# Kernel optimization log

Hardware: AMD Instinct MI355X
Metric: run time of the kernel (lower is better)

The kernel has to match this reference:

```python
import jax, jax.numpy as jnp
import numpy as np

D_MODEL = 1024
NUM_HEADS = 16
HEAD_DIM = D_MODEL // NUM_HEADS
B, S = 2, 2048


def setup_inputs() -> dict:
    key = jax.random.key(0)
    ks = jax.random.split(key, 12)
    s = 1.0 / np.sqrt(D_MODEL)
    return {
        "query": jax.random.normal(ks[0], (B, S, D_MODEL), jnp.float32),
        "key": jax.random.normal(ks[1], (B, S, D_MODEL), jnp.float32),
        "value": jax.random.normal(ks[2], (B, S, D_MODEL), jnp.float32),
        "attn_mask": jnp.ones((B, 1, 1, S), dtype=bool),
        "w_q": jax.random.uniform(ks[3], (D_MODEL, D_MODEL), jnp.float32, -s, s),
        "b_q": jax.random.uniform(ks[4], (D_MODEL,), jnp.float32, -s, s),
        "w_k": jax.random.uniform(ks[5], (D_MODEL, D_MODEL), jnp.float32, -s, s),
        "b_k": jax.random.uniform(ks[6], (D_MODEL,), jnp.float32, -s, s),
        "w_v": jax.random.uniform(ks[7], (D_MODEL, D_MODEL), jnp.float32, -s, s),
        "b_v": jax.random.uniform(ks[8], (D_MODEL,), jnp.float32, -s, s),
        "w_o": jax.random.uniform(ks[9], (D_MODEL, D_MODEL), jnp.float32, -s, s),
        "b_o": jax.random.uniform(ks[10], (D_MODEL,), jnp.float32, -s, s),
    }


def _split_heads(x):
    b, s, _ = x.shape
    return x.reshape(b, s, NUM_HEADS, HEAD_DIM).transpose(0, 2, 1, 3)  # [B,H,S,hd]


def reference(query, key, value, attn_mask, w_q, b_q, w_k, b_k, w_v, b_v, w_o, b_o):
    q = _split_heads(query @ w_q.T + b_q)
    k = _split_heads(key @ w_k.T + b_k)
    v = _split_heads(value @ w_v.T + b_v)
    scale = 1.0 / np.sqrt(HEAD_DIM).astype(np.float32)
    scores = jnp.einsum("bhqd,bhkd->bhqk", q, k) * scale  # [B,H,S,S]
    scores = jnp.where(attn_mask, scores, jnp.float32(-1e9))
    weights = jax.nn.softmax(scores, axis=-1)
    attended = jnp.einsum("bhqk,bhkd->bhqd", weights, v)
    merged = attended.transpose(0, 2, 1, 3).reshape(query.shape[0], query.shape[1], D_MODEL)
    return merged @ w_o.T + b_o
```

## Files before the change

kernel.cpp:

```cpp
#include <hip/hip_runtime.h>

#define D_MODEL 1024
#define NHEADS 16
#define HDIM 64
#define BATCH 2
#define SEQ 2048

typedef __attribute__((ext_vector_type(8))) short short8;
typedef __attribute__((ext_vector_type(4))) float floatx4;

__device__ __forceinline__ short f2bf(float f) {
    unsigned u = __builtin_bit_cast(unsigned, f);
    u += 0x7fffu + ((u >> 16) & 1u);
    return (short)(u >> 16);
}

#if defined(__has_builtin)
#if __has_builtin(__builtin_amdgcn_cvt_pk_bf16_f32)
#define HAS_PK_BF16 1
#endif
#if __has_builtin(__builtin_amdgcn_exp2f)
#define EXP2(x) __builtin_amdgcn_exp2f(x)
#endif
#endif
#ifndef EXP2
#define EXP2(x) exp2f(x)
#endif
__device__ __forceinline__ unsigned pk2bf(float a, float b) {
#ifdef HAS_PK_BF16
    auto r = __builtin_amdgcn_cvt_pk_bf16_f32(a, b);
    unsigned out;
    __builtin_memcpy(&out, &r, 4);
    return out;
#else
    unsigned ua = __builtin_bit_cast(unsigned, a);
    ua += 0x7fffu + ((ua >> 16) & 1u);
    unsigned ub = __builtin_bit_cast(unsigned, b);
    ub += 0x7fffu + ((ub >> 16) & 1u);
    return (ua >> 16) | (ub & 0xffff0000u);
#endif
}

__device__ __forceinline__ void gll16(const void* g, void* l) {
    __builtin_amdgcn_global_load_lds(
        (const __attribute__((address_space(1))) unsigned int*)g,
        (__attribute__((address_space(3))) unsigned int*)l, 16, 0, 0);
}

__global__ __launch_bounds__(256)
void cvt_all(const float* __restrict__ q, const float* __restrict__ k,
             const float* __restrict__ v, const float* __restrict__ wq,
             const float* __restrict__ wk, const float* __restrict__ wv,
             const float* __restrict__ wo, short* __restrict__ ws)
{
    const int seg = blockIdx.y;
    const float* src; short* dst; int n;
    const int M4 = 1 << 22, M1 = 1 << 20;
    switch (seg) {
        case 0: src = q;  dst = ws;                    n = M4; break;
        case 1: src = k;  dst = ws + M4;               n = M4; break;
        case 2: src = v;  dst = ws + 2 * M4;           n = M4; break;
        case 3: src = wq; dst = ws + 3 * M4;           n = M1; break;
        case 4: src = wk; dst = ws + 3 * M4 + M1;      n = M1; break;
        case 5: src = wv; dst = ws + 3 * M4 + 2 * M1;  n = M1; break;
        default:src = wo; dst = ws + 3 * M4 + 3 * M1;  n = M1; break;
    }
    int idx = (blockIdx.x * 256 + threadIdx.x) * 8;
    if (idx >= n) return;
    float4 f0 = *(const float4*)(src + idx);
    float4 f1 = *(const float4*)(src + idx + 4);
    uint4 o = { pk2bf(f0.x, f0.y), pk2bf(f0.z, f0.w),
                pk2bf(f1.x, f1.y), pk2bf(f1.z, f1.w) };
    *(uint4*)(dst + idx) = o;
}

template<int FINAL>
__global__ __launch_bounds__(256)
void gemm_pipe(const short* __restrict__ Abase, const short* __restrict__ Wbase,
               const float* __restrict__ b0, const float* __restrict__ b1,
               const float* __restrict__ b2, void* __restrict__ outp,
               float scale0)
{
    constexpr int BM = FINAL ? 64 : 128;
    constexpr int WM = FINAL ? 32 : 64;
    constexpr int MT = WM / 16;
    constexpr int AG = BM / 32;
    __shared__ short smem[BM * 64 + 128 * 64];
    short* As = smem;
    short* Bs = smem + BM * 64;

    const int tid  = threadIdx.x;
    const int lane = tid & 63;
    const int w    = tid >> 6;
    const int wr   = (w >> 1) * WM;
    const int wc   = (w & 1) * 64;
    const int m0   = blockIdx.y * BM;
    const int n0   = blockIdx.x * 128;
    const int z    = FINAL ? 0 : blockIdx.z;

    const short* A = Abase + (size_t)z * (1 << 22);
    const short* W = Wbase + (size_t)z * (1 << 20);
    const float* bias = FINAL ? b0 : (z == 0 ? b0 : (z == 1 ? b1 : b2));
    const float scale = (!FINAL && z == 0) ? scale0 : 1.0f;

    const int slr = lane >> 3;
    const int scb = (lane & 7) ^ slr;
    const int fm  = lane & 15;
    const int fq  = lane >> 4;

    const short* aSrc[AG];
    const short* bSrc[4];
#pragma unroll
    for (int i = 0; i < AG; ++i)
        aSrc[i] = A + (size_t)(m0 + (w * AG + i) * 8 + slr) * D_MODEL + scb * 8;
#pragma unroll
    for (int i = 0; i < 4; ++i)
        bSrc[i] = W + (size_t)(n0 + (w * 4 + i) * 8 + slr) * D_MODEL + scb * 8;

    short8 pa[AG], pb[4];
#pragma unroll
    for (int i = 0; i < AG; ++i) pa[i] = *(const short8*)(aSrc[i]);
#pragma unroll
    for (int i = 0; i < 4; ++i)  pb[i] = *(const short8*)(bSrc[i]);

    floatx4 acc[MT][4] = {};

    for (int k0 = 0; k0 < D_MODEL; k0 += 64) {
        __syncthreads();
#pragma unroll
        for (int i = 0; i < AG; ++i)
            *(short8*)(As + (w * AG + i) * 512 + lane * 8) = pa[i];
#pragma unroll
        for (int i = 0; i < 4; ++i)
            *(short8*)(Bs + (w * 4 + i) * 512 + lane * 8) = pb[i];
        const int kn = (k0 + 64) & (D_MODEL - 1);
#pragma unroll
        for (int i = 0; i < AG; ++i) pa[i] = *(const short8*)(aSrc[i] + kn);
#pragma unroll
        for (int i = 0; i < 4; ++i)  pb[i] = *(const short8*)(bSrc[i] + kn);
        __syncthreads();

#pragma unroll
        for (int ks = 0; ks < 2; ++ks) {
            short8 af[MT], bfv[4];
#pragma unroll
            for (int mt = 0; mt < MT; ++mt) {
                int row = wr + mt * 16 + fm;
                af[mt] = *(const short8*)(As + row * 64 + ((ks * 4 + fq) ^ (row & 7)) * 8);
            }
#pragma unroll
            for (int nt = 0; nt < 4; ++nt) {
                int row = wc + nt * 16 + fm;
                bfv[nt] = *(const short8*)(Bs + row * 64 + ((ks * 4 + fq) ^ (row & 7)) * 8);
            }
#pragma unroll
            for (int mt = 0; mt < MT; ++mt)
#pragma unroll
                for (int nt = 0; nt < 4; ++nt)
                    acc[mt][nt] = __builtin_amdgcn_mfma_f32_16x16x32_bf16(
                        af[mt], bfv[nt], acc[mt][nt], 0, 0, 0);
        }
    }

    if (!FINAL && z == 2) {
        __syncthreads();
        short* T = smem;
#pragma unroll
        for (int nt = 0; nt < 4; ++nt) {
            int nl = wc + nt * 16 + fm;
            float bv = bias[n0 + nl];
#pragma unroll
            for (int mt = 0; mt < MT; ++mt)
#pragma unroll
                for (int r = 0; r < 4; ++r) {
                    int m = wr + mt * 16 + fq * 4 + r;
                    int mp = (m & 64) | ((m & 15) << 2) | ((m >> 4) & 3);
                    T[nl * 128 + (((mp >> 3) ^ (nl & 15)) << 3) + (mp & 7)]
                        = f2bf(acc[mt][nt][r] + bv);
                }
        }
        __syncthreads();
        const int nl   = tid >> 1, half = tid & 1;
        const int gb   = m0 >> 11;
        const int gh   = (n0 + nl) >> 6, gd = (n0 + nl) & 63;
        const int ms   = m0 & 2047;
        short* gdst = (short*)outp + ((size_t)2 << 22)
                    + ((((size_t)(gb * NHEADS + gh)) << 6) + gd) * SEQ + ms;
#pragma unroll
        for (int c = 0; c < 8; ++c) {
            int lc = half * 8 + c;
            int p  = lc ^ (nl & 15);
            *(short8*)(gdst + lc * 8) = *(const short8*)(T + nl * 128 + p * 8);
        }
        return;
    }
#pragma unroll
    for (int nt = 0; nt < 4; ++nt) {
        int n = n0 + wc + nt * 16 + fm;
        float bv = bias[n];
#pragma unroll
        for (int mt = 0; mt < MT; ++mt) {
#pragma unroll
            for (int r = 0; r < 4; ++r) {
                int m = m0 + wr + mt * 16 + fq * 4 + r;
                float val = (acc[mt][nt][r] + bv) * scale;
                if (FINAL) {
                    ((float*)outp)[(size_t)m * D_MODEL + n] = val;
                } else {
                    short* outz = (short*)outp + (size_t)z * (1 << 22);
                    int b = m >> 11, s = m & 2047, h = n >> 6, d = n & 63;
                    outz[(((size_t)(b * NHEADS + h) * SEQ + s) << 6) + d] = f2bf(val);
                }
            }
        }
    }
}

__global__ __launch_bounds__(256, 4)
void flash5(const short* __restrict__ qh, const short* __restrict__ kh,
            const short* __restrict__ vT, short* __restrict__ ab)
{
    __shared__ short Ks[2 * 64 * 64];
    __shared__ short Vt[2 * 64 * 64];
    __shared__ short Ps[64 * 64];

    const int tid  = threadIdx.x;
    const int lane = tid & 63;
    const int w    = tid >> 6;
    const int wq0  = w * 16;
    const int bh   = blockIdx.y;
    const int b    = bh >> 4, h = bh & 15;
    const int s0   = blockIdx.x * 64;
    const size_t base = (size_t)bh << 17;

    const int fm = lane & 15;
    const int fq = lane >> 4;
    const int fk = fq * 8;

    short8 qf[2];
#pragma unroll
    for (int ks = 0; ks < 2; ++ks)
        qf[ks] = *(const short8*)(qh + base +
            (size_t)(s0 + wq0 + fm) * HDIM + ks * 32 + fk);

    const int slr = lane >> 3;
    const int lcb = (lane & 7) ^ slr;

    const short* kb0 = kh + base;
    const short* vb0 = vT + base;
    int kSo[2][2], vSo[2][2];
#pragma unroll
    for (int sub = 0; sub < 2; ++sub)
#pragma unroll
        for (int i = 0; i < 2; ++i) {
            int row = (w * 2 + i) * 8 + slr;
            kSo[sub][i] = (sub * 64 + row) * HDIM + lcb * 8;
            vSo[sub][i] = row * SEQ + sub * 64 + lcb * 8;
        }

    int off[2][4];
#pragma unroll
    for (int ks = 0; ks < 2; ++ks)
#pragma unroll
        for (int nt = 0; nt < 4; ++nt)
            off[ks][nt] = (nt * 16 + fm) * 64 + (((ks * 4 + fq) ^ (fm & 7)) * 8);
    int psr[2];
#pragma unroll
    for (int ks = 0; ks < 2; ++ks)
        psr[ks] = (wq0 + fm) * 64 + (((ks * 4 + fq) ^ (fm & 7)) * 8);
    int pw[4];
#pragma unroll
    for (int r = 0; r < 4; ++r) {
        int row = wq0 + fq * 4 + r;
        pw[r] = row * 64 + (((fm >> 1) ^ (row & 7)) << 3) + ((fm & 1) << 2);
    }
    int lw[2][2];
#pragma unroll
    for (int sub = 0; sub < 2; ++sub)
#pragma unroll
        for (int i = 0; i < 2; ++i)
            lw[sub][i] = sub * 4096 + (w * 2 + i) * 512 + lane * 8;

    const short8 ones = { 0x3f80, 0x3f80, 0x3f80, 0x3f80,
                          0x3f80, 0x3f80, 0x3f80, 0x3f80 };

    short8 pkv[2][2], pvv[2][2];
#pragma unroll
    for (int sub = 0; sub < 2; ++sub)
#pragma unroll
        for (int i = 0; i < 2; ++i) {
            pkv[sub][i] = *(const short8*)(kb0 + kSo[sub][i]);
            pvv[sub][i] = *(const short8*)(vb0 + vSo[sub][i]);
        }

    floatx4 O[4] = {};
    floatx4 accL = {};

    for (int kt = 0; kt < SEQ; kt += 128) {
        __syncthreads();
#pragma unroll
        for (int sub = 0; sub < 2; ++sub)
#pragma unroll
            for (int i = 0; i < 2; ++i) {
                *(short8*)(Ks + lw[sub][i]) = pkv[sub][i];
                *(short8*)(Vt + lw[sub][i]) = pvv[sub][i];
            }
        const int kn = (kt + 128) & (SEQ - 1);
#pragma unroll
        for (int sub = 0; sub < 2; ++sub)
#pragma unroll
            for (int i = 0; i < 2; ++i) {
                pkv[sub][i] = *(const short8*)(kb0 + kSo[sub][i] + kn * HDIM);
                pvv[sub][i] = *(const short8*)(vb0 + vSo[sub][i] + kn);
            }
        __syncthreads();

#pragma unroll
        for (int sub = 0; sub < 2; ++sub) {
            const short* Kb = Ks + sub * 4096;
            const short* Vb = Vt + sub * 4096;

            floatx4 sc[4] = {};
#pragma unroll
            for (int ks = 0; ks < 2; ++ks) {
                short8 bfv[4];
#pragma unroll
                for (int nt = 0; nt < 4; ++nt)
                    bfv[nt] = *(const short8*)(Kb + off[ks][nt]);
                __builtin_amdgcn_s_setprio(1);
#pragma unroll
                for (int nt = 0; nt < 4; ++nt)
                    sc[nt] = __builtin_amdgcn_mfma_f32_16x16x32_bf16(
                        qf[ks], bfv[nt], sc[nt], 0, 0, 0);
                __builtin_amdgcn_s_setprio(0);
            }

#pragma unroll
            for (int r = 0; r < 4; ++r) {
                float p0 = EXP2(sc[0][r]);
                float p1 = EXP2(sc[1][r]);
                float p2 = EXP2(sc[2][r]);
                float p3 = EXP2(sc[3][r]);
                uint2 pv = { pk2bf(p0, p1), pk2bf(p2, p3) };
                *(uint2*)(Ps + pw[r]) = pv;
            }

#pragma unroll
            for (int ks = 0; ks < 2; ++ks) {
                short8 af = *(const short8*)(Ps + psr[ks]);
                short8 bfv[4];
#pragma unroll
                for (int nt = 0; nt < 4; ++nt)
                    bfv[nt] = *(const short8*)(Vb + off[ks][nt]);
                __builtin_amdgcn_s_setprio(1);
                accL = __builtin_amdgcn_mfma_f32_16x16x32_bf16(af, ones, accL, 0, 0, 0);
#pragma unroll
                for (int nt = 0; nt < 4; ++nt)
                    O[nt] = __builtin_amdgcn_mfma_f32_16x16x32_bf16(
                        af, bfv[nt], O[nt], 0, 0, 0);
                __builtin_amdgcn_s_setprio(0);
            }
        }
    }

#pragma unroll
    for (int r = 0; r < 4; ++r) {
        float inv = 1.0f / accL[r];
        int s = s0 + wq0 + fq * 4 + r;
        short* orow = ab + (((size_t)(b * SEQ + s) * NHEADS + h) << 6);
#pragma unroll
        for (int nt = 0; nt < 4; ++nt)
            orow[nt * 16 + fm] = f2bf(O[nt][r] * inv);
    }
}

extern "C" void kernel_launch(void* const* d_in, const int* in_sizes, int n_in,
                              void* d_out, int out_size, void* d_ws, size_t ws_size,
                              hipStream_t stream) {
    const float* query = (const float*)d_in[0];
    const float* key_  = (const float*)d_in[1];
    const float* value = (const float*)d_in[2];
    const float* bq = (const float*)d_in[5];
    const float* bk = (const float*)d_in[7];
    const float* bv = (const float*)d_in[9];
    const float* bo = (const float*)d_in[11];
    float* out = (float*)d_out;

    const int M4 = 1 << 22, M1 = 1 << 20;
    short* ws  = (short*)d_ws;
    short* qx  = ws;
    short* wqb = ws + 3 * M4;
    short* wob = wqb + 3 * M1;
    short* qh  = ws + 4 * M4;
    short* khd = ws + 5 * M4;
    short* vTh = ws + 6 * M4;
    short* ab  = ws + 7 * M4;

    const float SCALE = 0.125f * 1.44269504088896340736f;

    dim3 blk(256);
    cvt_all<<<dim3(2048, 7), blk, 0, stream>>>(
        query, key_, value, (const float*)d_in[4], (const float*)d_in[6],
        (const float*)d_in[8], (const float*)d_in[10], ws);

    gemm_pipe<0><<<dim3(D_MODEL / 128, (BATCH * SEQ) / 128, 3), blk, 0, stream>>>(
        qx, wqb, bq, bk, bv, qh, SCALE);

    flash5<<<dim3(SEQ / 64, BATCH * NHEADS), blk, 0, stream>>>(qh, khd, vTh, ab);

    gemm_pipe<1><<<dim3(D_MODEL / 128, (BATCH * SEQ) / 64), blk, 0, stream>>>(
        ab, wob, bo, bo, bo, out, 1.0f);
}
```

Baseline: 229.4 us.

## Double-buffer K/V register prefetch and remap block ids for L2 locality

The flash attention loop now keeps two register sets of K/V prefetches, so global loads are issued two 128-key tiles ahead instead of one, which hides more load latency. Block ids are also linearised and remapped so that consecutively scheduled blocks spread across batch-heads in a fixed pattern, aiming for better L2/XCD locality of K/V. The cost is extra VGPRs for the second prefetch buffer, which could reduce occupancy under the 4-wave launch bound. The remap also assumes a specific grid shape.

```diff
diff --git a/kernel.cpp b/kernel.cpp
--- a/kernel.cpp
+++ b/kernel.cpp
@@ -228,9 +228,10 @@
     const int lane = tid & 63;
     const int w    = tid >> 6;
     const int wq0  = w * 16;
-    const int bh   = blockIdx.y;
+    const int id   = blockIdx.y * gridDim.x + blockIdx.x;
+    const int bh   = (id & 7) * 4 + (id >> 8);
+    const int s0   = ((id >> 3) & 31) * 64;
     const int b    = bh >> 4, h = bh & 15;
-    const int s0   = blockIdx.x * 64;
     const size_t base = (size_t)bh << 17;
 
     const int fm = lane & 15;
@@ -284,37 +285,28 @@
     const short8 ones = { 0x3f80, 0x3f80, 0x3f80, 0x3f80,
                           0x3f80, 0x3f80, 0x3f80, 0x3f80 };
 
-    short8 pkv[2][2], pvv[2][2];
-#pragma unroll
-    for (int sub = 0; sub < 2; ++sub)
-#pragma unroll
-        for (int i = 0; i < 2; ++i) {
-            pkv[sub][i] = *(const short8*)(kb0 + kSo[sub][i]);
-            pvv[sub][i] = *(const short8*)(vb0 + vSo[sub][i]);
-        }
-
     floatx4 O[4] = {};
     floatx4 accL = {};
 
-    for (int kt = 0; kt < SEQ; kt += 128) {
-        __syncthreads();
+    auto issue = [&](short8 (&pk)[2][2], short8 (&pv)[2][2], int kn) {
 #pragma unroll
         for (int sub = 0; sub < 2; ++sub)
 #pragma unroll
             for (int i = 0; i < 2; ++i) {
-                *(short8*)(Ks + lw[sub][i]) = pkv[sub][i];
-                *(short8*)(Vt + lw[sub][i]) = pvv[sub][i];
-            }
-        const int kn = (kt + 128) & (SEQ - 1);
+                pk[sub][i] = *(const short8*)(kb0 + kSo[sub][i] + kn * HDIM);
+                pv[sub][i] = *(const short8*)(vb0 + vSo[sub][i] + kn);
+            }
+    };
+    auto commit = [&](short8 (&pk)[2][2], short8 (&pv)[2][2]) {
 #pragma unroll
         for (int sub = 0; sub < 2; ++sub)
 #pragma unroll
             for (int i = 0; i < 2; ++i) {
-                pkv[sub][i] = *(const short8*)(kb0 + kSo[sub][i] + kn * HDIM);
-                pvv[sub][i] = *(const short8*)(vb0 + vSo[sub][i] + kn);
-            }
-        __syncthreads();
-
+                *(short8*)(Ks + lw[sub][i]) = pk[sub][i];
+                *(short8*)(Vt + lw[sub][i]) = pv[sub][i];
+            }
+    };
+    auto compute = [&]() {
 #pragma unroll
         for (int sub = 0; sub < 2; ++sub) {
             const short* Kb = Ks + sub * 4096;
@@ -361,6 +353,23 @@
                 __builtin_amdgcn_s_setprio(0);
             }
         }
+    };
+
+    short8 kA[2][2], vA[2][2], kB[2][2], vB[2][2];
+    issue(kA, vA, 0);
+    issue(kB, vB, 128);
+
+    for (int kt = 0; kt < SEQ; kt += 256) {
+        __syncthreads();
+        commit(kA, vA);
+        issue(kA, vA, (kt + 256) & (SEQ - 1));
+        __syncthreads();
+        compute();
+        __syncthreads();
+        commit(kB, vB);
+        issue(kB, vB, (kt + 384) & (SEQ - 1));
+        __syncthreads();
+        compute();
     }
 
 #pragma unroll
```

New measurement: 281.0 us. +22.5%, slower.
